# Optimization experiments

Measured on AMD Instinct MI355X. Metric: run time of the kernel, lower is better.

## Reference

```python
import jax, jax.numpy as jnp
import numpy as np

WH, WW = 8, 8          # window size
NH = 8                 # num heads
ED = 256               # embed dim
HD = ED // NH          # head dim
SCALE = HD ** -0.5


def setup_inputs() -> dict:
    key = jax.random.key(0)
    k1, k2, k3, k4 = jax.random.split(key, 4)
    x = jax.random.normal(k1, (8, ED, 128, 128), dtype=jnp.float32)
    w_qkv = jax.random.normal(k2, (3 * ED, ED), dtype=jnp.float32) * (ED ** -0.5)
    w_out = jax.random.normal(k3, (ED, ED), dtype=jnp.float32) * (ED ** -0.5)
    b_out = jax.random.normal(k4, (ED,), dtype=jnp.float32) * 0.01
    return {"x": x, "w_qkv": w_qkv, "w_out": w_out, "b_out": b_out}


def reference(x, w_qkv, w_out, b_out):
    # x: [B, C, H, W] (NCHW) -> [B, H, W, C]
    x = jnp.transpose(x, (0, 2, 3, 1))
    B, H, W, C = x.shape
    pad_h = (WH - H % WH) % WH
    pad_w = (WW - W % WW) % WW
    x = jnp.pad(x, ((0, 0), (0, pad_h), (0, pad_w), (0, 0)))
    Hp, Wp = H + pad_h, W + pad_w
    nh, nw = Hp // WH, Wp // WW
    N = WH * WW
    # window partition -> [B*nh*nw, N, C]
    xw = x.reshape(B, nh, WH, nw, WW, C).transpose(0, 1, 3, 2, 4, 5).reshape(-1, N, C)
    # qkv projection (no bias): [nW, N, 3, NH, HD]
    qkv = (xw @ w_qkv.T).reshape(-1, N, 3, NH, HD)
    q, k, v = qkv[:, :, 0], qkv[:, :, 1], qkv[:, :, 2]  # [nW, N, NH, HD]
    # NOTE: faithful to source — attention across the HEADS axis per token
    attn = jnp.einsum('wnhd,wngd->wnhg', q, k) * SCALE  # [nW, N, NH, NH]
    attn = jax.nn.softmax(attn, axis=-1)
    out = jnp.einsum('wnhg,wngd->wnhd', attn, v)        # [nW, N, NH, HD]
    # torch: transpose(1,2).reshape(-1, N, C)
    out = out.transpose(0, 2, 1, 3).reshape(-1, N, C)
    out = out @ w_out.T + b_out
    # window merge
    out = out.reshape(B, nh, nw, WH, WW, C).transpose(0, 1, 3, 2, 4, 5).reshape(B, Hp, Wp, C)
    out = out[:, :H, :W, :]
    # faithful final permute(0,3,2,1): [B, C, W, H]
    return jnp.transpose(out, (0, 3, 2, 1))
```

## Files before the change

### kernel.cpp

```cpp
#include <hip/hip_runtime.h>

#define SCALE 0.17677669529663687f

typedef __attribute__((ext_vector_type(8))) short bf16x8;
typedef __attribute__((ext_vector_type(4))) float f32x4;

__device__ __forceinline__ unsigned short f2bf(float f) {
    unsigned u = __float_as_uint(f);
    u += 0x7FFFu + ((u >> 16) & 1u);
    return (unsigned short)(u >> 16);
}
__device__ __forceinline__ float bf2f(unsigned short s) {
    return __uint_as_float(((unsigned)s) << 16);
}
__device__ __forceinline__ unsigned pk2c(float a, float b) {
    return (unsigned)f2bf(a) | ((unsigned)f2bf(b) << 16);
}

__global__ __launch_bounds__(256) void wconv_kernel(
        const float* __restrict__ w_qkv, const float* __restrict__ w_out,
        unsigned short* __restrict__ wq, unsigned short* __restrict__ wo) {
    int idx = blockIdx.x * 256 + threadIdx.x;
    if (idx < 196608) wq[idx] = f2bf(w_qkv[idx]);
    else if (idx < 262144) wo[idx - 196608] = f2bf(w_out[idx - 196608]);
}

__global__ __launch_bounds__(1024, 4) void qkv_attn_fused64_kernel(
        const float* __restrict__ x, const unsigned short* __restrict__ wq,
        unsigned short* __restrict__ o_ws) {
    extern __shared__ unsigned char lds[];
    const int tid = threadIdx.x;
    const int tb  = blockIdx.x << 6;
    const int b   = tb >> 14;
    const float* xb = x + (size_t)b * 4194304 + (tb & 16383);

    {
        const int tok   = tid & 63;
        const int cbase = (tid >> 6) * 16;
        float f[16];
        #pragma unroll
        for (int e = 0; e < 16; ++e)
            f[e] = xb[(size_t)(cbase + e) * 16384 + tok];
        #pragma unroll
        for (int hlf = 0; hlf < 2; ++hlf) {
            const int c0 = cbase + hlf * 8;
            unsigned u0 = pk2c(f[hlf*8+0], f[hlf*8+1]), u1 = pk2c(f[hlf*8+2], f[hlf*8+3]);
            unsigned u2 = pk2c(f[hlf*8+4], f[hlf*8+5]), u3 = pk2c(f[hlf*8+6], f[hlf*8+7]);
            const int slot = (c0 >> 3) ^ (tok & 7);
            *(uint4*)(lds + tok * 512 + (slot << 4)) = make_uint4(u0, u1, u2, u3);
        }
    }
    __syncthreads();

    const int lane = tid & 63;
    const int wave = tid >> 6;
    const int lrow = lane & 15, lk = lane >> 4;
    const int j0w = wave * 48;

    f32x4 acc[4][3];
    #pragma unroll
    for (int mt = 0; mt < 4; ++mt)
        #pragma unroll
        for (int nt = 0; nt < 3; ++nt)
            acc[mt][nt] = (f32x4){0.f, 0.f, 0.f, 0.f};
    #pragma unroll
    for (int k = 0; k < 8; ++k) {
        bf16x8 a[4], bb[3];
        #pragma unroll
        for (int mt = 0; mt < 4; ++mt) {
            int t = mt * 16 + lrow;
            int slot = (k * 4 + lk) ^ (t & 7);
            a[mt] = *(const bf16x8*)(lds + t * 512 + (slot << 4));
        }
        #pragma unroll
        for (int nt = 0; nt < 3; ++nt) {
            int j = j0w + nt * 16 + lrow;
            bb[nt] = *(const bf16x8*)((const unsigned char*)wq + (size_t)j * 512 + k * 64 + lk * 16);
        }
        #pragma unroll
        for (int mt = 0; mt < 4; ++mt)
            #pragma unroll
            for (int nt = 0; nt < 3; ++nt)
                acc[mt][nt] = __builtin_amdgcn_mfma_f32_16x16x32_bf16(a[mt], bb[nt], acc[mt][nt], 0, 0, 0);
    }
    #pragma unroll
    for (int mt = 0; mt < 4; ++mt)
        #pragma unroll
        for (int nt = 0; nt < 3; ++nt)
            #pragma unroll
            for (int i = 0; i < 4; ++i) {
                int t = mt * 16 + lk * 4 + i;
                int ch = j0w + nt * 16 + lrow;
                int slot = (ch >> 3) ^ (t & 7);
                *(unsigned short*)(lds + 32768 + t * 1536 + (slot << 4) + (ch & 7) * 2) = f2bf(acc[mt][nt][i]);
            }
    __syncthreads();

    {
        const int t  = tid >> 4;
        const int h  = (tid >> 1) & 7;
        const int hf = tid & 1;
        const int tx = t & 7;
        const unsigned char* row = lds + 32768 + t * 1536;
        float q[16];
        #pragma unroll
        for (int jj = 0; jj < 2; ++jj) {
            int slot = (h * 4 + hf * 2 + jj) ^ tx;
            bf16x8 v = *(const bf16x8*)(row + (slot << 4));
            #pragma unroll
            for (int e = 0; e < 8; ++e) q[jj * 8 + e] = bf2f((unsigned short)v[e]);
        }
        float dots[8];
        #pragma unroll
        for (int g = 0; g < 8; ++g) {
            float acc2 = 0.f;
            #pragma unroll
            for (int jj = 0; jj < 2; ++jj) {
                int slot = (32 + g * 4 + hf * 2 + jj) ^ tx;
                bf16x8 v = *(const bf16x8*)(row + (slot << 4));
                #pragma unroll
                for (int e = 0; e < 8; ++e) acc2 += q[jj * 8 + e] * bf2f((unsigned short)v[e]);
            }
            dots[g] = acc2;
        }
        #pragma unroll
        for (int g = 0; g < 8; ++g)
            dots[g] = (dots[g] + __shfl_xor(dots[g], 1, 64)) * SCALE;
        float mx = dots[0];
        #pragma unroll
        for (int g = 1; g < 8; ++g) mx = fmaxf(mx, dots[g]);
        float sum = 0.f;
        #pragma unroll
        for (int g = 0; g < 8; ++g) { dots[g] = __expf(dots[g] - mx); sum += dots[g]; }
        const float inv = 1.f / sum;
        float o[16];
        #pragma unroll
        for (int d = 0; d < 16; ++d) o[d] = 0.f;
        #pragma unroll
        for (int g = 0; g < 8; ++g) {
            const float p = dots[g] * inv;
            #pragma unroll
            for (int jj = 0; jj < 2; ++jj) {
                int slot = (64 + g * 4 + hf * 2 + jj) ^ tx;
                bf16x8 v = *(const bf16x8*)(row + (slot << 4));
                #pragma unroll
                for (int e = 0; e < 8; ++e) o[jj * 8 + e] += p * bf2f((unsigned short)v[e]);
            }
        }
        const int tok = tb + t;
        const int bb2 = tok >> 14, rem = tok & 16383;
        const int himg = rem >> 7, wimg = rem & 127;
        const int ih = himg >> 3, r = himg & 7;
        const int iw = wimg >> 3, s = wimg & 7;
        const int win = (bb2 << 8) + (ih << 4) + iw;
        unsigned short* dst = o_ws + ((size_t)win * 64 + h * 8 + r) * 256 + s * 32 + hf * 16;
        #pragma unroll
        for (int jj = 0; jj < 2; ++jj) {
            uint4 v = make_uint4(pk2c(o[jj * 8 + 0], o[jj * 8 + 1]), pk2c(o[jj * 8 + 2], o[jj * 8 + 3]),
                                 pk2c(o[jj * 8 + 4], o[jj * 8 + 5]), pk2c(o[jj * 8 + 6], o[jj * 8 + 7]));
            *(uint4*)(dst + jj * 8) = v;
        }
    }
}

__global__ __launch_bounds__(512, 4) void qkv_attn_fused_kernel(
        const float* __restrict__ x, const unsigned short* __restrict__ wq,
        unsigned short* __restrict__ o_ws) {
    __shared__ unsigned char lds[65536];
    const int tid = threadIdx.x;
    const int tb  = blockIdx.x << 5;
    const int b   = tb >> 14;
    const float* xb = x + (size_t)b * 4194304 + (tb & 16383);

    {
        const int tok   = tid & 31;
        const int cbase = (tid >> 5) * 16;
        float f[16];
        #pragma unroll
        for (int e = 0; e < 16; ++e)
            f[e] = xb[(size_t)(cbase + e) * 16384 + tok];
        #pragma unroll
        for (int hlf = 0; hlf < 2; ++hlf) {
            const int c0 = cbase + hlf * 8;
            unsigned u0 = pk2c(f[hlf*8+0], f[hlf*8+1]), u1 = pk2c(f[hlf*8+2], f[hlf*8+3]);
            unsigned u2 = pk2c(f[hlf*8+4], f[hlf*8+5]), u3 = pk2c(f[hlf*8+6], f[hlf*8+7]);
            const int slot = (c0 >> 3) ^ (tok & 7);
            *(uint4*)(lds + tok * 512 + (slot << 4)) = make_uint4(u0, u1, u2, u3);
        }
    }
    __syncthreads();

    const int lane = tid & 63;
    const int wave = tid >> 6;
    const int lrow = lane & 15, lk = lane >> 4;
    const int j0w = wave * 96;

    f32x4 acc[2][6];
    #pragma unroll
    for (int mt = 0; mt < 2; ++mt)
        #pragma unroll
        for (int nt = 0; nt < 6; ++nt)
            acc[mt][nt] = (f32x4){0.f, 0.f, 0.f, 0.f};
    #pragma unroll
    for (int k = 0; k < 8; ++k) {
        bf16x8 a[2], bb[6];
        #pragma unroll
        for (int mt = 0; mt < 2; ++mt) {
            int t = mt * 16 + lrow;
            int slot = (k * 4 + lk) ^ (t & 7);
            a[mt] = *(const bf16x8*)(lds + t * 512 + (slot << 4));
        }
        #pragma unroll
        for (int nt = 0; nt < 6; ++nt) {
            int j = j0w + nt * 16 + lrow;
            bb[nt] = *(const bf16x8*)((const unsigned char*)wq + (size_t)j * 512 + k * 64 + lk * 16);
        }
        #pragma unroll
        for (int mt = 0; mt < 2; ++mt)
            #pragma unroll
            for (int nt = 0; nt < 6; ++nt)
                acc[mt][nt] = __builtin_amdgcn_mfma_f32_16x16x32_bf16(a[mt], bb[nt], acc[mt][nt], 0, 0, 0);
    }
    #pragma unroll
    for (int mt = 0; mt < 2; ++mt)
        #pragma unroll
        for (int nt = 0; nt < 6; ++nt)
            #pragma unroll
            for (int i = 0; i < 4; ++i) {
                int t = mt * 16 + lk * 4 + i;
                int ch = j0w + nt * 16 + lrow;
                int slot = (ch >> 3) ^ (t & 7);
                *(unsigned short*)(lds + 16384 + t * 1536 + (slot << 4) + (ch & 7) * 2) = f2bf(acc[mt][nt][i]);
            }
    __syncthreads();

    {
        const int t  = tid >> 4;
        const int h  = (tid >> 1) & 7;
        const int hf = tid & 1;
        const int tx = t & 7;
        const unsigned char* row = lds + 16384 + t * 1536;
        float q[16];
        #pragma unroll
        for (int jj = 0; jj < 2; ++jj) {
            int slot = (h * 4 + hf * 2 + jj) ^ tx;
            bf16x8 v = *(const bf16x8*)(row + (slot << 4));
            #pragma unroll
            for (int e = 0; e < 8; ++e) q[jj * 8 + e] = bf2f((unsigned short)v[e]);
        }
        float dots[8];
        #pragma unroll
        for (int g = 0; g < 8; ++g) {
            float acc2 = 0.f;
            #pragma unroll
            for (int jj = 0; jj < 2; ++jj) {
                int slot = (32 + g * 4 + hf * 2 + jj) ^ tx;
                bf16x8 v = *(const bf16x8*)(row + (slot << 4));
                #pragma unroll
                for (int e = 0; e < 8; ++e) acc2 += q[jj * 8 + e] * bf2f((unsigned short)v[e]);
            }
            dots[g] = acc2;
        }
        #pragma unroll
        for (int g = 0; g < 8; ++g)
            dots[g] = (dots[g] + __shfl_xor(dots[g], 1, 64)) * SCALE;
        float mx = dots[0];
        #pragma unroll
        for (int g = 1; g < 8; ++g) mx = fmaxf(mx, dots[g]);
        float sum = 0.f;
        #pragma unroll
        for (int g = 0; g < 8; ++g) { dots[g] = __expf(dots[g] - mx); sum += dots[g]; }
        const float inv = 1.f / sum;
        float o[16];
        #pragma unroll
        for (int d = 0; d < 16; ++d) o[d] = 0.f;
        #pragma unroll
        for (int g = 0; g < 8; ++g) {
            const float p = dots[g] * inv;
            #pragma unroll
            for (int jj = 0; jj < 2; ++jj) {
                int slot = (64 + g * 4 + hf * 2 + jj) ^ tx;
                bf16x8 v = *(const bf16x8*)(row + (slot << 4));
                #pragma unroll
                for (int e = 0; e < 8; ++e) o[jj * 8 + e] += p * bf2f((unsigned short)v[e]);
            }
        }
        const int tok = tb + t;
        const int bb2 = tok >> 14, rem = tok & 16383;
        const int himg = rem >> 7, wimg = rem & 127;
        const int ih = himg >> 3, r = himg & 7;
        const int iw = wimg >> 3, s = wimg & 7;
        const int win = (bb2 << 8) + (ih << 4) + iw;
        unsigned short* dst = o_ws + ((size_t)win * 64 + h * 8 + r) * 256 + s * 32 + hf * 16;
        #pragma unroll
        for (int jj = 0; jj < 2; ++jj) {
            uint4 v = make_uint4(pk2c(o[jj * 8 + 0], o[jj * 8 + 1]), pk2c(o[jj * 8 + 2], o[jj * 8 + 3]),
                                 pk2c(o[jj * 8 + 4], o[jj * 8 + 5]), pk2c(o[jj * 8 + 6], o[jj * 8 + 7]));
            *(uint4*)(dst + jj * 8) = v;
        }
    }
}

__global__ __launch_bounds__(512, 6) void outproj_kernel(
        const unsigned short* __restrict__ o_ws, const unsigned short* __restrict__ wo,
        const float* __restrict__ b_out, float* __restrict__ out) {
    __shared__ unsigned char lds[32768];
    const int tid = threadIdx.x;
    const int bid = blockIdx.x;
    const int b  = bid >> 8;
    const int ih = (bid >> 4) & 15;
    const int iw = bid & 15;

    {
        const unsigned char* src = (const unsigned char*)(o_ws + (size_t)bid * 16384);
        #pragma unroll
        for (int it = 0; it < 4; ++it) {
            int q = it * 512 + tid;
            int np = q >> 5;
            int slot = (q & 31) ^ (np & 7);
            *(bf16x8*)(lds + np * 512 + (slot << 4)) = *(const bf16x8*)(src + q * 16);
        }
    }
    __syncthreads();

    const int lane = tid & 63;
    const int wave = tid >> 6;
    const int lrow = lane & 15;
    const int lk   = lane >> 4;
    const int j0 = wave * 32;

    f32x4 acc[4][2];
    #pragma unroll
    for (int mt = 0; mt < 4; ++mt)
        #pragma unroll
        for (int nt = 0; nt < 2; ++nt)
            acc[mt][nt] = (f32x4){0.f, 0.f, 0.f, 0.f};
    #pragma unroll
    for (int k = 0; k < 8; ++k) {
        bf16x8 a[4], bb[2];
        #pragma unroll
        for (int mt = 0; mt < 4; ++mt) {
            int t = mt * 16 + lrow;
            int slot = (k * 4 + lk) ^ (t & 7);
            a[mt] = *(const bf16x8*)(lds + t * 512 + (slot << 4));
        }
        #pragma unroll
        for (int nt = 0; nt < 2; ++nt) {
            int j = j0 + nt * 16 + lrow;
            bb[nt] = *(const bf16x8*)((const unsigned char*)wo + (size_t)j * 512 + k * 64 + lk * 16);
        }
        #pragma unroll
        for (int mt = 0; mt < 4; ++mt)
            #pragma unroll
            for (int nt = 0; nt < 2; ++nt)
                acc[mt][nt] = __builtin_amdgcn_mfma_f32_16x16x32_bf16(a[mt], bb[nt], acc[mt][nt], 0, 0, 0);
    }
    float bias[2];
    #pragma unroll
    for (int nt = 0; nt < 2; ++nt) bias[nt] = b_out[j0 + nt * 16 + lrow];
    __syncthreads();

    const size_t obase = ((size_t)b * 256) * 16384 + (size_t)(iw * 8) * 128 + ih * 8;
    #pragma unroll
    for (int half = 0; half < 2; ++half) {
        if ((wave >> 2) == half) {
            int jl = (wave & 3) * 32;
            #pragma unroll
            for (int mt = 0; mt < 4; ++mt)
                #pragma unroll
                for (int nt = 0; nt < 2; ++nt)
                    #pragma unroll
                    for (int i = 0; i < 4; ++i) {
                        int t = mt * 16 + lk * 4 + i;
                        int el = jl + nt * 16 + lrow;
                        int sl = (el >> 2) ^ (t & 7);
                        *(float*)(lds + t * 512 + (sl << 4) + (el & 3) * 4) = acc[mt][nt][i] + bias[nt];
                    }
        }
        __syncthreads();
        #pragma unroll
        for (int it = 0; it < 2; ++it) {
            int idx = it * 512 + tid;
            int el = idx >> 3, sp = idx & 7;
            float vals[8];
            #pragma unroll
            for (int rp = 0; rp < 8; ++rp) {
                int t = rp * 8 + sp;
                int sl = (el >> 2) ^ (t & 7);
                vals[rp] = *(const float*)(lds + t * 512 + (sl << 4) + (el & 3) * 4);
            }
            float* po = out + obase + (size_t)(half * 128 + el) * 16384 + sp * 128;
            *(float4*)po       = make_float4(vals[0], vals[1], vals[2], vals[3]);
            *(float4*)(po + 4) = make_float4(vals[4], vals[5], vals[6], vals[7]);
        }
        __syncthreads();
    }
}

extern "C" void kernel_launch(void* const* d_in, const int* in_sizes, int n_in,
                              void* d_out, int out_size, void* d_ws, size_t ws_size,
                              hipStream_t stream) {
    const float* x     = (const float*)d_in[0];
    const float* w_qkv = (const float*)d_in[1];
    const float* w_out = (const float*)d_in[2];
    const float* b_out = (const float*)d_in[3];
    float* out = (float*)d_out;

    const size_t O_BYTES = 67108864;

    unsigned short* o_ws = (unsigned short*)d_ws;
    unsigned short* wq   = (unsigned short*)((char*)d_ws + O_BYTES);
    unsigned short* wo   = wq + 196608;

    wconv_kernel<<<dim3(1024), dim3(256), 0, stream>>>(w_qkv, w_out, wq, wo);

    hipError_t aerr = hipFuncSetAttribute(
        reinterpret_cast<const void*>(qkv_attn_fused64_kernel),
        hipFuncAttributeMaxDynamicSharedMemorySize, 131072);
    if (aerr == hipSuccess) {
        qkv_attn_fused64_kernel<<<dim3(2048), dim3(1024), 131072, stream>>>(x, wq, o_ws);
    } else {
        qkv_attn_fused_kernel<<<dim3(4096), dim3(512), 0, stream>>>(x, wq, o_ws);
    }

    outproj_kernel<<<dim3(2048), dim3(512), 0, stream>>>(o_ws, wo, b_out, out);
}
```

Baseline: 235.2 us.

## Fuse output projection into per-window QKV-attention kernel

Each block now processes one 8x8 spatial window rather than 64 consecutive row tokens. It keeps the attention output in LDS, runs the output-projection MFMA GEMM in place, and writes the transposed final output directly. This removes the bf16 intermediate round trip through global memory and the separate outproj kernel launch. The risks are lower occupancy from the larger LDS footprint, extra syncs, and input loads that are only 8 floats contiguous per window row.

```diff
diff --git a/kernel.cpp b/kernel.cpp
--- a/kernel.cpp
+++ b/kernel.cpp
@@ -25,22 +25,26 @@
     else if (idx < 262144) wo[idx - 196608] = f2bf(w_out[idx - 196608]);
 }
 
-__global__ __launch_bounds__(1024, 4) void qkv_attn_fused64_kernel(
+__global__ __launch_bounds__(1024, 4) void mega_kernel(
         const float* __restrict__ x, const unsigned short* __restrict__ wq,
-        unsigned short* __restrict__ o_ws) {
+        const unsigned short* __restrict__ wo, const float* __restrict__ b_out,
+        float* __restrict__ out) {
     extern __shared__ unsigned char lds[];
     const int tid = threadIdx.x;
-    const int tb  = blockIdx.x << 6;
-    const int b   = tb >> 14;
-    const float* xb = x + (size_t)b * 4194304 + (tb & 16383);
-
-    {
-        const int tok   = tid & 63;
+    const int bid = blockIdx.x;
+    const int b  = bid >> 8;
+    const int ih = (bid >> 4) & 15;
+    const int iw = bid & 15;
+    const float* xb = x + (size_t)b * 4194304 + (size_t)(ih * 8) * 128 + iw * 8;
+
+    {
+        const int tok = tid & 63;
+        const int r = tok >> 3, s = tok & 7;
         const int cbase = (tid >> 6) * 16;
         float f[16];
         #pragma unroll
         for (int e = 0; e < 16; ++e)
-            f[e] = xb[(size_t)(cbase + e) * 16384 + tok];
+            f[e] = xb[(size_t)(cbase + e) * 16384 + r * 128 + s];
         #pragma unroll
         for (int hlf = 0; hlf < 2; ++hlf) {
             const int c0 = cbase + hlf * 8;
@@ -55,45 +59,47 @@
     const int lane = tid & 63;
     const int wave = tid >> 6;
     const int lrow = lane & 15, lk = lane >> 4;
-    const int j0w = wave * 48;
-
-    f32x4 acc[4][3];
-    #pragma unroll
-    for (int mt = 0; mt < 4; ++mt)
-        #pragma unroll
-        for (int nt = 0; nt < 3; ++nt)
-            acc[mt][nt] = (f32x4){0.f, 0.f, 0.f, 0.f};
-    #pragma unroll
-    for (int k = 0; k < 8; ++k) {
-        bf16x8 a[4], bb[3];
-        #pragma unroll
-        for (int mt = 0; mt < 4; ++mt) {
-            int t = mt * 16 + lrow;
-            int slot = (k * 4 + lk) ^ (t & 7);
-            a[mt] = *(const bf16x8*)(lds + t * 512 + (slot << 4));
-        }
-        #pragma unroll
-        for (int nt = 0; nt < 3; ++nt) {
-            int j = j0w + nt * 16 + lrow;
-            bb[nt] = *(const bf16x8*)((const unsigned char*)wq + (size_t)j * 512 + k * 64 + lk * 16);
-        }
+
+    {
+        const int j0w = wave * 48;
+        f32x4 acc[4][3];
         #pragma unroll
         for (int mt = 0; mt < 4; ++mt)
             #pragma unroll
             for (int nt = 0; nt < 3; ++nt)
-                acc[mt][nt] = __builtin_amdgcn_mfma_f32_16x16x32_bf16(a[mt], bb[nt], acc[mt][nt], 0, 0, 0);
-    }
-    #pragma unroll
-    for (int mt = 0; mt < 4; ++mt)
-        #pragma unroll
-        for (int nt = 0; nt < 3; ++nt)
-            #pragma unroll
-            for (int i = 0; i < 4; ++i) {
-                int t = mt * 16 + lk * 4 + i;
-                int ch = j0w + nt * 16 + lrow;
-                int slot = (ch >> 3) ^ (t & 7);
-                *(unsigned short*)(lds + 32768 + t * 1536 + (slot << 4) + (ch & 7) * 2) = f2bf(acc[mt][nt][i]);
-            }
+                acc[mt][nt] = (f32x4){0.f, 0.f, 0.f, 0.f};
+        #pragma unroll
+        for (int k = 0; k < 8; ++k) {
+            bf16x8 a[4], bb[3];
+            #pragma unroll
+            for (int mt = 0; mt < 4; ++mt) {
+                int t = mt * 16 + lrow;
+                int slot = (k * 4 + lk) ^ (t & 7);
+                a[mt] = *(const bf16x8*)(lds + t * 512 + (slot << 4));
+            }
+            #pragma unroll
+            for (int nt = 0; nt < 3; ++nt) {
+                int j = j0w + nt * 16 + lrow;
+                bb[nt] = *(const bf16x8*)((const unsigned char*)wq + (size_t)j * 512 + k * 64 + lk * 16);
+            }
+            #pragma unroll
+            for (int mt = 0; mt < 4; ++mt)
+                #pragma unroll
+                for (int nt = 0; nt < 3; ++nt)
+                    acc[mt][nt] = __builtin_amdgcn_mfma_f32_16x16x32_bf16(a[mt], bb[nt], acc[mt][nt], 0, 0, 0);
+        }
+        #pragma unroll
+        for (int mt = 0; mt < 4; ++mt)
+            #pragma unroll
+            for (int nt = 0; nt < 3; ++nt)
+                #pragma unroll
+                for (int i = 0; i < 4; ++i) {
+                    int t = mt * 16 + lk * 4 + i;
+                    int ch = j0w + nt * 16 + lrow;
+                    int slot = (ch >> 3) ^ (t & 7);
+                    *(unsigned short*)(lds + 32768 + t * 1536 + (slot << 4) + (ch & 7) * 2) = f2bf(acc[mt][nt][i]);
+                }
+    }
     __syncthreads();
 
     {
@@ -147,18 +153,67 @@
                 for (int e = 0; e < 8; ++e) o[jj * 8 + e] += p * bf2f((unsigned short)v[e]);
             }
         }
-        const int tok = tb + t;
-        const int bb2 = tok >> 14, rem = tok & 16383;
-        const int himg = rem >> 7, wimg = rem & 127;
-        const int ih = himg >> 3, r = himg & 7;
-        const int iw = wimg >> 3, s = wimg & 7;
-        const int win = (bb2 << 8) + (ih << 4) + iw;
-        unsigned short* dst = o_ws + ((size_t)win * 64 + h * 8 + r) * 256 + s * 32 + hf * 16;
+        const int np = h * 8 + (t >> 3);
+        const int s  = t & 7;
         #pragma unroll
         for (int jj = 0; jj < 2; ++jj) {
+            const int c = s * 4 + hf * 2 + jj;
             uint4 v = make_uint4(pk2c(o[jj * 8 + 0], o[jj * 8 + 1]), pk2c(o[jj * 8 + 2], o[jj * 8 + 3]),
                                  pk2c(o[jj * 8 + 4], o[jj * 8 + 5]), pk2c(o[jj * 8 + 6], o[jj * 8 + 7]));
-            *(uint4*)(dst + jj * 8) = v;
+            *(uint4*)(lds + np * 512 + ((c ^ (np & 7)) << 4)) = v;
+        }
+    }
+    __syncthreads();
+
+    {
+        const int j0 = wave * 16;
+        f32x4 acc2[4];
+        #pragma unroll
+        for (int mt = 0; mt < 4; ++mt) acc2[mt] = (f32x4){0.f, 0.f, 0.f, 0.f};
+        #pragma unroll
+        for (int k = 0; k < 8; ++k) {
+            bf16x8 a[4], bbo;
+            #pragma unroll
+            for (int mt = 0; mt < 4; ++mt) {
+                int t = mt * 16 + lrow;
+                int slot = (k * 4 + lk) ^ (t & 7);
+                a[mt] = *(const bf16x8*)(lds + t * 512 + (slot << 4));
+            }
+            bbo = *(const bf16x8*)((const unsigned char*)wo + (size_t)(j0 + lrow) * 512 + k * 64 + lk * 16);
+            #pragma unroll
+            for (int mt = 0; mt < 4; ++mt)
+                acc2[mt] = __builtin_amdgcn_mfma_f32_16x16x32_bf16(a[mt], bbo, acc2[mt], 0, 0, 0);
+        }
+        const float bias = b_out[j0 + lrow];
+        __syncthreads();
+        #pragma unroll
+        for (int mt = 0; mt < 4; ++mt)
+            #pragma unroll
+            for (int i = 0; i < 4; ++i) {
+                int t2 = mt * 16 + lk * 4 + i;
+                int e  = j0 + lrow;
+                int sl = (e >> 2) ^ (t2 & 7);
+                *(float*)(lds + 32768 + t2 * 1024 + (sl << 4) + (e & 3) * 4) = acc2[mt][i] + bias;
+            }
+    }
+    __syncthreads();
+
+    {
+        const size_t obase = ((size_t)b * 256) * 16384 + (size_t)(iw * 8) * 128 + ih * 8;
+        #pragma unroll
+        for (int it = 0; it < 2; ++it) {
+            int idx = it * 1024 + tid;
+            int el = idx >> 3, sp = idx & 7;
+            float vals[8];
+            #pragma unroll
+            for (int rp = 0; rp < 8; ++rp) {
+                int t = rp * 8 + sp;
+                int sl = (el >> 2) ^ (t & 7);
+                vals[rp] = *(const float*)(lds + 32768 + t * 1024 + (sl << 4) + (el & 3) * 4);
+            }
+            float* po = out + obase + (size_t)el * 16384 + sp * 128;
+            *(float4*)po       = make_float4(vals[0], vals[1], vals[2], vals[3]);
+            *(float4*)(po + 4) = make_float4(vals[4], vals[5], vals[6], vals[7]);
         }
     }
 }
@@ -415,13 +470,12 @@
     wconv_kernel<<<dim3(1024), dim3(256), 0, stream>>>(w_qkv, w_out, wq, wo);
 
     hipError_t aerr = hipFuncSetAttribute(
-        reinterpret_cast<const void*>(qkv_attn_fused64_kernel),
+        reinterpret_cast<const void*>(mega_kernel),
         hipFuncAttributeMaxDynamicSharedMemorySize, 131072);
     if (aerr == hipSuccess) {
-        qkv_attn_fused64_kernel<<<dim3(2048), dim3(1024), 131072, stream>>>(x, wq, o_ws);
+        mega_kernel<<<dim3(2048), dim3(1024), 131072, stream>>>(x, wq, wo, b_out, out);
     } else {
         qkv_attn_fused_kernel<<<dim3(4096), dim3(512), 0, stream>>>(x, wq, o_ws);
-    }
-
-    outproj_kernel<<<dim3(2048), dim3(512), 0, stream>>>(o_ws, wo, b_out, out);
-}
+        outproj_kernel<<<dim3(2048), dim3(512), 0, stream>>>(o_ws, wo, b_out, out);
+    }
+}
```

Measured after the change: 268.9 us. 14.3% more time.
